# Kernel optimization log

Hardware: AMD Instinct MI355X
Metric: run time of the kernel (lower is better)

The kernel has to match this reference:

```python
import jax, jax.numpy as jnp
import numpy as np

POS_THR = 0.01
EXPANSION = 0.3
HW_RATIO = 2.0


def setup_inputs() -> dict:
    key = jax.random.key(0)
    kp, kj, kv, kg, km = jax.random.split(key, 5)
    B, P, K, H, W = 16, 20, 17, 160, 160
    hm_pred = jax.random.uniform(kp, (B, K, H, W), dtype=jnp.float32)  # some above POS_THR
    gt = jax.random.uniform(kg, (B, K, H, W), dtype=jnp.float32)
    xy = jax.random.uniform(kj, (B, P, K, 2), dtype=jnp.float32) * jnp.array([W, H], jnp.float32)
    v = (jax.random.uniform(kv, (B, P, K, 1)) > 0.3).astype(jnp.float32)
    jointsXYV = jnp.concatenate([xy, v], axis=-1)
    masks = (jax.random.uniform(km, (B, H, W)) > 0.02).astype(jnp.float32)
    return {"hm_pred": hm_pred, "jointsXYV": jointsXYV, "masks": masks, "gt": gt}


def _gen_hm_mask(hm_pred, masks, jointsXYV):
    # hm_pred: [B,K,H,W]; masks: [B,H,W]; jointsXYV: [B,P,K,3]
    B, K, H, W = hm_pred.shape
    f32 = hm_pred.dtype
    vis = (jointsXYV[..., 2] > 0).any(axis=2)          # [B,P] person has any visible joint
    invisible = jointsXYV[..., 2] <= 0                 # [B,P,K]
    xy = jointsXYV[..., :2]                            # [B,P,K,2]
    inf = jnp.asarray(jnp.inf, f32)
    bb_TL = jnp.where(invisible[..., None], inf, xy).min(axis=2)    # [B,P,2]
    bb_BR = jnp.where(invisible[..., None], -inf, xy).max(axis=2)   # [B,P,2]
    bb_WH = jnp.maximum(bb_BR - bb_TL, 1.0)
    bb_CT = 0.5 * (bb_BR + bb_TL)
    bb_WH = jnp.maximum(bb_WH, bb_WH[..., ::-1] / HW_RATIO)
    half = (0.5 + EXPANSION) * bb_WH
    BR = jnp.round(bb_CT + half)
    TL = jnp.round(bb_CT - half)
    gy = jnp.arange(H, dtype=f32)[:, None]             # [H,1]
    gx = jnp.arange(W, dtype=f32)[None, :]             # [1,W]
    minx = TL[..., 0][:, :, None, None]
    miny = TL[..., 1][:, :, None, None]
    maxx = BR[..., 0][:, :, None, None]
    maxy = BR[..., 1][:, :, None, None]
    # True outside the person's expanded bbox  [B,P,H,W]
    outside = (gx < minx) | (gx > maxx) | (gy < miny) | (gy > maxy)
    # per-person per-keypoint mask: 1 keeps pixel; 0 suppresses inside-bbox pixels of
    # invisible keypoints. [B,P,K,H,W]
    paf = outside[:, :, None, :, :] | (~invisible)[:, :, :, None, None]
    # persons with no visible joint were filtered by nonzero() in torch -> neutral (all True)
    paf = paf | (~vis)[:, :, None, None, None]
    allp = paf.all(axis=1)                             # min-reduce over persons  [B,K,H,W]
    hm_masks = jnp.minimum(masks[:, None, :, :], allp.astype(f32))
    hm_masks = jnp.where(hm_pred >= POS_THR, jnp.asarray(1.0, f32), hm_masks)
    return hm_masks


def reference(hm_pred, jointsXYV, masks, gt):
    hm_masks = _gen_hm_mask(hm_pred, masks, jointsXYV)
    loss = (hm_pred - gt) ** 2 * hm_masks
    return loss.mean(axis=(1, 2, 3))  # per-image loss [B]
```

## Files before the change

kernel.cpp:

```cpp
#include <hip/hip_runtime.h>

#define BB 16
#define PP 20
#define KK 17
#define HH 160
#define WW 160
#define PIX (HH * WW)
#define TPB 64
#define VPT 4
#define PIXPERBLK (TPB * VPT)
#define BLKPERB (PIX / PIXPERBLK)
#define NBLK (BB * BLKPERB)
#define POS_THR 0.01f

struct Person {
    float minx, miny, maxx, maxy;
    unsigned int active;
    unsigned int invmask;
};


__global__ void __launch_bounds__(TPB) main_kernel(
        const float* __restrict__ hm, const float* __restrict__ gt,
        const float* __restrict__ masks, const float* __restrict__ joints,
        float* __restrict__ out) {
    __shared__ Person sP[PP];
    int b = blockIdx.x / BLKPERB;
    int blk = blockIdx.x % BLKPERB;

    if (threadIdx.x < PP) {
        const float* j = joints + ((size_t)b * PP + threadIdx.x) * KK * 3;
        float tlx = INFINITY, tly = INFINITY, brx = -INFINITY, bry = -INFINITY;
        unsigned int inv = 0;
        bool anyvis = false;
        #pragma unroll
        for (int k = 0; k < KK; ++k) {
            float x = j[k * 3 + 0];
            float y = j[k * 3 + 1];
            float v = j[k * 3 + 2];
            if (v > 0.0f) {
                anyvis = true;
                tlx = fminf(tlx, x); tly = fminf(tly, y);
                brx = fmaxf(brx, x); bry = fmaxf(bry, y);
            } else {
                inv |= (1u << k);
            }
        }
        Person ps;
        if (!anyvis) {
            ps.active = 0; ps.invmask = 0;
            ps.minx = 0.0f; ps.miny = 0.0f; ps.maxx = -1.0f; ps.maxy = -1.0f;
        } else {
            float w0 = fmaxf(brx - tlx, 1.0f);
            float h0 = fmaxf(bry - tly, 1.0f);
            float cx = 0.5f * (brx + tlx);
            float cy = 0.5f * (bry + tly);
            float w1 = fmaxf(w0, h0 / 2.0f);
            float h1 = fmaxf(h0, w0 / 2.0f);
            float hx = (0.5f + 0.3f) * w1;
            float hy = (0.5f + 0.3f) * h1;
            ps.minx = rintf(cx - hx);
            ps.maxx = rintf(cx + hx);
            ps.miny = rintf(cy - hy);
            ps.maxy = rintf(cy + hy);
            ps.active = 1;
            ps.invmask = inv;
        }
        sP[threadIdx.x] = ps;
    }
    __syncthreads();

    int pix0 = blk * PIXPERBLK + threadIdx.x * VPT;
    float gy = (float)(pix0 / WW);
    int x0 = pix0 % WW;

    unsigned int jm0 = 0, jm1 = 0, jm2 = 0, jm3 = 0;
    #pragma unroll
    for (int p = 0; p < PP; ++p) {
        Person ps = sP[p];
        bool iy = (ps.active != 0u) & (gy >= ps.miny) & (gy <= ps.maxy);
        if (iy) {
            float fx0 = (float)x0;
            if ((fx0 >= ps.minx)        & (fx0 <= ps.maxx))        jm0 |= ps.invmask;
            if ((fx0 + 1.0f >= ps.minx) & (fx0 + 1.0f <= ps.maxx)) jm1 |= ps.invmask;
            if ((fx0 + 2.0f >= ps.minx) & (fx0 + 2.0f <= ps.maxx)) jm2 |= ps.invmask;
            if ((fx0 + 3.0f >= ps.minx) & (fx0 + 3.0f <= ps.maxx)) jm3 |= ps.invmask;
        }
    }

    const float4* m4 = (const float4*)(masks + (size_t)b * PIX);
    float4 mv = m4[pix0 >> 2];

    float lsum = 0.0f;
    const size_t planeBase = (size_t)b * KK * PIX;
    #pragma unroll
    for (int k = 0; k < KK; ++k) {
        const float4* h4 = (const float4*)(hm + planeBase + (size_t)k * PIX);
        const float4* g4 = (const float4*)(gt + planeBase + (size_t)k * PIX);
        float4 h = h4[pix0 >> 2];
        float4 g = g4[pix0 >> 2];
        float a0 = ((jm0 >> k) & 1u) ? 0.0f : 1.0f;
        float a1 = ((jm1 >> k) & 1u) ? 0.0f : 1.0f;
        float a2 = ((jm2 >> k) & 1u) ? 0.0f : 1.0f;
        float a3 = ((jm3 >> k) & 1u) ? 0.0f : 1.0f;
        float m0 = (h.x >= POS_THR) ? 1.0f : fminf(mv.x, a0);
        float m1 = (h.y >= POS_THR) ? 1.0f : fminf(mv.y, a1);
        float m2 = (h.z >= POS_THR) ? 1.0f : fminf(mv.z, a2);
        float m3 = (h.w >= POS_THR) ? 1.0f : fminf(mv.w, a3);
        float d0 = h.x - g.x, d1 = h.y - g.y, d2 = h.z - g.z, d3 = h.w - g.w;
        lsum = fmaf(d0 * d0, m0, lsum);
        lsum = fmaf(d1 * d1, m1, lsum);
        lsum = fmaf(d2 * d2, m2, lsum);
        lsum = fmaf(d3 * d3, m3, lsum);
    }

    #pragma unroll
    for (int off = 32; off > 0; off >>= 1) lsum += __shfl_down(lsum, off);
    if (threadIdx.x == 0) {
        atomicAdd(&out[b], lsum / (float)(KK * HH * WW));
    }
}

extern "C" void kernel_launch(void* const* d_in, const int* in_sizes, int n_in,
                              void* d_out, int out_size, void* d_ws, size_t ws_size,
                              hipStream_t stream) {
    const float* hm     = (const float*)d_in[0];
    const float* joints = (const float*)d_in[1];
    const float* masks  = (const float*)d_in[2];
    const float* gt     = (const float*)d_in[3];
    float* out = (float*)d_out;

    main_kernel<<<NBLK, TPB, 0, stream>>>(hm, gt, masks, joints, out);
}
```

Before: 114.1 us.

## Split joint-mask precompute into separate kernel and stream contiguous segments in main loss

Per-pixel keypoint suppression masks are now computed once per image by a separate kernel and written to workspace as uint4 bitmasks. The main kernel then has 512-thread blocks each walk a contiguous segment of the flattened K×H×W planes, reloading mask and bitmask data per quad, and does a two-level block reduction so there are fewer atomics. The aim is better streaming coalescing and fewer, larger blocks with less redundant person-box work. The cost is an extra kernel launch, a round trip of the workspace through global memory, and extra mask and bitmask reads for every keypoint plane.

```diff
diff --git a/kernel.cpp b/kernel.cpp
--- a/kernel.cpp
+++ b/kernel.cpp
@@ -6,11 +6,9 @@
 #define HH 160
 #define WW 160
 #define PIX (HH * WW)
-#define TPB 64
-#define VPT 4
-#define PIXPERBLK (TPB * VPT)
-#define BLKPERB (PIX / PIXPERBLK)
-#define NBLK (BB * BLKPERB)
+#define QPP (PIX / 4)
+#define QPB_TOTAL (KK * QPP)
+#define SEG_QUADS 6800
 #define POS_THR 0.01f
 
 struct Person {
@@ -20,14 +18,8 @@
 };
 
 
-__global__ void __launch_bounds__(TPB) main_kernel(
-        const float* __restrict__ hm, const float* __restrict__ gt,
-        const float* __restrict__ masks, const float* __restrict__ joints,
-        float* __restrict__ out) {
-    __shared__ Person sP[PP];
-    int b = blockIdx.x / BLKPERB;
-    int blk = blockIdx.x % BLKPERB;
-
+__device__ __forceinline__ void prep_persons(const float* __restrict__ joints,
+                                             int b, Person* sP) {
     if (threadIdx.x < PP) {
         const float* j = joints + ((size_t)b * PP + threadIdx.x) * KK * 3;
         float tlx = INFINITY, tly = INFINITY, brx = -INFINITY, bry = -INFINITY;
@@ -68,11 +60,21 @@
         }
         sP[threadIdx.x] = ps;
     }
+}
+
+__global__ void __launch_bounds__(256) jmask_kernel(const float* __restrict__ joints,
+                                                    uint4* __restrict__ jm4) {
+    __shared__ Person sP[PP];
+    const int b   = blockIdx.x / 25;
+    const int seg = blockIdx.x % 25;
+    prep_persons(joints, b, sP);
     __syncthreads();
 
-    int pix0 = blk * PIXPERBLK + threadIdx.x * VPT;
-    float gy = (float)(pix0 / WW);
-    int x0 = pix0 % WW;
+    const int q = seg * 256 + threadIdx.x;
+    const int y = q / 40;
+    const int x0 = (q - y * 40) * 4;
+    const float gy = (float)y;
+    const float fx0 = (float)x0;
 
     unsigned int jm0 = 0, jm1 = 0, jm2 = 0, jm3 = 0;
     #pragma unroll
@@ -80,44 +82,87 @@
         Person ps = sP[p];
         bool iy = (ps.active != 0u) & (gy >= ps.miny) & (gy <= ps.maxy);
         if (iy) {
-            float fx0 = (float)x0;
             if ((fx0 >= ps.minx)        & (fx0 <= ps.maxx))        jm0 |= ps.invmask;
             if ((fx0 + 1.0f >= ps.minx) & (fx0 + 1.0f <= ps.maxx)) jm1 |= ps.invmask;
             if ((fx0 + 2.0f >= ps.minx) & (fx0 + 2.0f <= ps.maxx)) jm2 |= ps.invmask;
             if ((fx0 + 3.0f >= ps.minx) & (fx0 + 3.0f <= ps.maxx)) jm3 |= ps.invmask;
         }
     }
+    uint4 r; r.x = jm0; r.y = jm1; r.z = jm2; r.w = jm3;
+    jm4[b * QPP + q] = r;
+}
 
-    const float4* m4 = (const float4*)(masks + (size_t)b * PIX);
-    float4 mv = m4[pix0 >> 2];
+__device__ __forceinline__ float quadloss(float4 h, float4 t, float4 m, uint4 jm, int k) {
+    float a0 = ((jm.x >> k) & 1u) ? 0.0f : 1.0f;
+    float a1 = ((jm.y >> k) & 1u) ? 0.0f : 1.0f;
+    float a2 = ((jm.z >> k) & 1u) ? 0.0f : 1.0f;
+    float a3 = ((jm.w >> k) & 1u) ? 0.0f : 1.0f;
+    float m0 = (h.x >= POS_THR) ? 1.0f : fminf(m.x, a0);
+    float m1 = (h.y >= POS_THR) ? 1.0f : fminf(m.y, a1);
+    float m2 = (h.z >= POS_THR) ? 1.0f : fminf(m.z, a2);
+    float m3 = (h.w >= POS_THR) ? 1.0f : fminf(m.w, a3);
+    float d0 = h.x - t.x, d1 = h.y - t.y, d2 = h.z - t.z, d3 = h.w - t.w;
+    float s = d0 * d0 * m0;
+    s = fmaf(d1 * d1, m1, s);
+    s = fmaf(d2 * d2, m2, s);
+    s = fmaf(d3 * d3, m3, s);
+    return s;
+}
+
+__global__ void __launch_bounds__(512) main_kernel(
+        const float* __restrict__ hm, const float* __restrict__ gt,
+        const float* __restrict__ masks, const uint4* __restrict__ jm4,
+        float* __restrict__ out) {
+    const int b   = blockIdx.x >> 4;
+    const int seg = blockIdx.x & 15;
+    const float4* __restrict__ hm4 = (const float4*)hm;
+    const float4* __restrict__ gt4 = (const float4*)gt;
+    const float4* __restrict__ mk4 = (const float4*)masks;
+
+    const size_t blkBase = (size_t)blockIdx.x * SEG_QUADS;
+    const int segBase = seg * SEG_QUADS;
+    const int mBase   = b * QPP;
 
     float lsum = 0.0f;
-    const size_t planeBase = (size_t)b * KK * PIX;
     #pragma unroll
-    for (int k = 0; k < KK; ++k) {
-        const float4* h4 = (const float4*)(hm + planeBase + (size_t)k * PIX);
-        const float4* g4 = (const float4*)(gt + planeBase + (size_t)k * PIX);
-        float4 h = h4[pix0 >> 2];
-        float4 g = g4[pix0 >> 2];
-        float a0 = ((jm0 >> k) & 1u) ? 0.0f : 1.0f;
-        float a1 = ((jm1 >> k) & 1u) ? 0.0f : 1.0f;
-        float a2 = ((jm2 >> k) & 1u) ? 0.0f : 1.0f;
-        float a3 = ((jm3 >> k) & 1u) ? 0.0f : 1.0f;
-        float m0 = (h.x >= POS_THR) ? 1.0f : fminf(mv.x, a0);
-        float m1 = (h.y >= POS_THR) ? 1.0f : fminf(mv.y, a1);
-        float m2 = (h.z >= POS_THR) ? 1.0f : fminf(mv.z, a2);
-        float m3 = (h.w >= POS_THR) ? 1.0f : fminf(mv.w, a3);
-        float d0 = h.x - g.x, d1 = h.y - g.y, d2 = h.z - g.z, d3 = h.w - g.w;
-        lsum = fmaf(d0 * d0, m0, lsum);
-        lsum = fmaf(d1 * d1, m1, lsum);
-        lsum = fmaf(d2 * d2, m2, lsum);
-        lsum = fmaf(d3 * d3, m3, lsum);
+    for (int gu = 0; gu < 7; ++gu) {
+        int i0 = gu * 1024 + threadIdx.x;
+        int i1 = i0 + 512;
+        bool v1 = (i1 < SEG_QUADS);
+        int i1c = v1 ? i1 : i0;
+
+        int qb0 = segBase + i0;
+        int k0 = qb0 / QPP;
+        int q0 = qb0 - k0 * QPP;
+        int qb1 = segBase + i1c;
+        int k1 = qb1 / QPP;
+        int q1 = qb1 - k1 * QPP;
+
+        float4 h0 = hm4[blkBase + i0];
+        float4 t0 = gt4[blkBase + i0];
+        float4 h1 = hm4[blkBase + i1c];
+        float4 t1 = gt4[blkBase + i1c];
+        float4 m0 = mk4[mBase + q0];
+        uint4  j0 = jm4[mBase + q0];
+        float4 m1 = mk4[mBase + q1];
+        uint4  j1 = jm4[mBase + q1];
+
+        lsum += quadloss(h0, t0, m0, j0, k0);
+        float c1 = quadloss(h1, t1, m1, j1, k1);
+        lsum += v1 ? c1 : 0.0f;
     }
 
     #pragma unroll
     for (int off = 32; off > 0; off >>= 1) lsum += __shfl_down(lsum, off);
+    __shared__ float wsum[8];
+    int lane = threadIdx.x & 63;
+    int wid  = threadIdx.x >> 6;
+    if (lane == 0) wsum[wid] = lsum;
+    __syncthreads();
     if (threadIdx.x == 0) {
-        atomicAdd(&out[b], lsum / (float)(KK * HH * WW));
+        float s = ((wsum[0] + wsum[1]) + (wsum[2] + wsum[3]))
+                + ((wsum[4] + wsum[5]) + (wsum[6] + wsum[7]));
+        atomicAdd(&out[b], s / (float)(KK * HH * WW));
     }
 }
 
@@ -129,6 +174,8 @@
     const float* masks  = (const float*)d_in[2];
     const float* gt     = (const float*)d_in[3];
     float* out = (float*)d_out;
+    uint4* jm4 = (uint4*)d_ws;
 
-    main_kernel<<<NBLK, TPB, 0, stream>>>(hm, gt, masks, joints, out);
+    jmask_kernel<<<BB * 25, 256, 0, stream>>>(joints, jm4);
+    main_kernel<<<BB * 16, 512, 0, stream>>>(hm, gt, masks, jm4, out);
 }
```

Result: faster. 106.7 us (-6.5%).
